# Kernel optimization log

Measured on AMD Instinct MI355X. Metric: run time of the kernel, lower is better.

The kernel has to match this reference:

```python
import jax, jax.numpy as jnp
import numpy as np

N_NODES = 100000
N_EDGES = 1600000
IN_FEATS = 128
OUT_FEATS = 64
NUM_HEADS = 1
K_HOPS = 3
NEG_SLOPE = 0.2


def setup_inputs() -> dict:
    key = jax.random.key(0)
    kf, kw, kl, kr, ks, kd = jax.random.split(key, 6)
    feat = jax.random.normal(kf, (N_NODES, IN_FEATS), dtype=jnp.float32)
    # xavier-normal-ish scaling (gain for relu ~ sqrt(2))
    W = jax.random.normal(kw, (OUT_FEATS * NUM_HEADS, IN_FEATS), dtype=jnp.float32) * np.sqrt(2.0 / (IN_FEATS + OUT_FEATS * NUM_HEADS))
    attn_l = jax.random.normal(kl, (1, NUM_HEADS, OUT_FEATS), dtype=jnp.float32) * 0.1
    attn_r = jax.random.normal(kr, (1, NUM_HEADS, OUT_FEATS), dtype=jnp.float32) * 0.1
    src = jax.random.randint(ks, (N_EDGES,), 0, N_NODES, dtype=jnp.int32)
    dst = jax.random.randint(kd, (N_EDGES,), 0, N_NODES, dtype=jnp.int32)
    return {"feat": feat, "W": W, "attn_l": attn_l, "attn_r": attn_r, "src": src, "dst": dst}


def _edge_softmax(e, dst, n_nodes):
    # e: [E, H, 1]; softmax over incoming edges of each dst node
    emax = jax.ops.segment_max(e, dst, num_segments=n_nodes)  # [N, H, 1]
    ee = jnp.exp(e - emax[dst])
    denom = jax.ops.segment_sum(ee, dst, num_segments=n_nodes)
    return ee / denom[dst]


def reference(feat, W, attn_l, attn_r, src, dst):
    n = feat.shape[0]
    h = (feat @ W.T).reshape(n, NUM_HEADS, OUT_FEATS)  # [N, H, F]
    el = jnp.sum(h * attn_l, axis=-1, keepdims=True)   # [N, H, 1]
    er = jnp.sum(h * attn_r, axis=-1, keepdims=True)   # [N, H, 1]
    e = el[src] + er[dst]                               # [E, H, 1]
    e = jnp.where(e > 0, e, NEG_SLOPE * e)              # leaky_relu
    a = _edge_softmax(e, dst, n)                        # [E, H, 1]

    ones = jnp.ones((src.shape[0],), dtype=feat.dtype)
    out_deg = jax.ops.segment_sum(ones, src, num_segments=n)
    in_deg = jax.ops.segment_sum(ones, dst, num_segments=n)
    out_norm = jnp.power(jnp.clip(out_deg, 1.0, None), -0.5)[:, None, None]  # deg^-0.5
    in_norm = jnp.power(jnp.clip(in_deg, 1.0, None), 0.5)[:, None, None]     # deg^+0.5 (as in source)

    feat_src = h
    for _ in range(K_HOPS):
        feat_src = feat_src * out_norm
        m = feat_src[src] * a                            # [E, H, F]
        feat_src = jax.ops.segment_sum(m, dst, num_segments=n)
        feat_src = feat_src * in_norm
    return feat_src  # [N, H, F]
```

## Files before the change

### kernel.cpp

```cpp
#include <hip/hip_runtime.h>
#include <hip/hip_fp16.h>
#include <math.h>

#define N_NODES 100000
#define N_EDGES 1600000
#define IN_F 128
#define OUT_F 64
#define NEG_SLOPE 0.2f

#define NBUCK 391
#define PB 512
#define EPB (N_EDGES / PB)

#define FS 132

typedef __attribute__((ext_vector_type(8))) short short8;
typedef __attribute__((ext_vector_type(4))) float f32x4;

__device__ __forceinline__ unsigned pack_bf(float f) {
    unsigned u  = __float_as_uint(f);
    unsigned hi = u & 0xffff0000u;
    float    lo = f - __uint_as_float(hi);
    return hi | (__float_as_uint(lo) >> 16);
}

__device__ __forceinline__ void unpack8(uint4 p0, uint4 p1, short8& hi, short8& lo) {
    hi[0] = (short)(p0.x >> 16); lo[0] = (short)(p0.x & 0xffffu);
    hi[1] = (short)(p0.y >> 16); lo[1] = (short)(p0.y & 0xffffu);
    hi[2] = (short)(p0.z >> 16); lo[2] = (short)(p0.z & 0xffffu);
    hi[3] = (short)(p0.w >> 16); lo[3] = (short)(p0.w & 0xffffu);
    hi[4] = (short)(p1.x >> 16); lo[4] = (short)(p1.x & 0xffffu);
    hi[5] = (short)(p1.y >> 16); lo[5] = (short)(p1.y & 0xffffu);
    hi[6] = (short)(p1.z >> 16); lo[6] = (short)(p1.z & 0xffffu);
    hi[7] = (short)(p1.w >> 16); lo[7] = (short)(p1.w & 0xffffu);
}

__global__ __launch_bounds__(256) void k_gemm(
        const float* __restrict__ feat, const float* __restrict__ W,
        const float* __restrict__ attn_l, const float* __restrict__ attn_r,
        __half* __restrict__ h16, float* __restrict__ el, float* __restrict__ er) {
    __shared__ __align__(16) unsigned flds[64 * FS];
    __shared__ __align__(16) unsigned wlds[64 * FS];
    int t = threadIdx.x;
    int n0 = blockIdx.x * 64;

    #pragma unroll
    for (int j = 0; j < 8; ++j) {
        int idx = t + j * 256;
        int row = idx >> 5, k4 = (idx & 31) * 4;
        float4 wv = *(const float4*)&W[row * IN_F + k4];
        unsigned* wp = &wlds[row * FS + k4];
        wp[0] = pack_bf(wv.x); wp[1] = pack_bf(wv.y);
        wp[2] = pack_bf(wv.z); wp[3] = pack_bf(wv.w);
        int g = n0 + row;
        float4 fv = {0.f, 0.f, 0.f, 0.f};
        if (g < N_NODES) fv = *(const float4*)&feat[(size_t)g * IN_F + k4];
        unsigned* fp = &flds[row * FS + k4];
        fp[0] = pack_bf(fv.x); fp[1] = pack_bf(fv.y);
        fp[2] = pack_bf(fv.z); fp[3] = pack_bf(fv.w);
    }
    __syncthreads();

    int lane = t & 63, wv_ = t >> 6;
    int quad = lane >> 4, nl = lane & 15;
    int mrow = wv_ * 16 + nl;

    f32x4 acc[4];
    #pragma unroll
    for (int nt = 0; nt < 4; ++nt) acc[nt] = (f32x4){0.f, 0.f, 0.f, 0.f};

    #pragma unroll
    for (int ks = 0; ks < 4; ++ks) {
        int ko = ks * 32 + quad * 8;
        const uint4* ap = (const uint4*)&flds[mrow * FS + ko];
        uint4 a0 = ap[0], a1 = ap[1];
        short8 ahi, alo; unpack8(a0, a1, ahi, alo);
        #pragma unroll
        for (int nt = 0; nt < 4; ++nt) {
            const uint4* bp = (const uint4*)&wlds[(nt * 16 + nl) * FS + ko];
            uint4 b0 = bp[0], b1 = bp[1];
            short8 bhi, blo; unpack8(b0, b1, bhi, blo);
            acc[nt] = __builtin_amdgcn_mfma_f32_16x16x32_bf16(ahi, bhi, acc[nt], 0, 0, 0);
            acc[nt] = __builtin_amdgcn_mfma_f32_16x16x32_bf16(ahi, blo, acc[nt], 0, 0, 0);
            acc[nt] = __builtin_amdgcn_mfma_f32_16x16x32_bf16(alo, bhi, acc[nt], 0, 0, 0);
        }
    }

    float al4[4], ar4[4];
    #pragma unroll
    for (int nt = 0; nt < 4; ++nt) { al4[nt] = attn_l[nt * 16 + nl]; ar4[nt] = attn_r[nt * 16 + nl]; }
    float elp[4] = {0.f, 0.f, 0.f, 0.f}, erp[4] = {0.f, 0.f, 0.f, 0.f};
    #pragma unroll
    for (int nt = 0; nt < 4; ++nt)
        #pragma unroll
        for (int r = 0; r < 4; ++r) {
            elp[r] += acc[nt][r] * al4[nt];
            erp[r] += acc[nt][r] * ar4[nt];
        }
    #pragma unroll
    for (int off = 1; off <= 8; off <<= 1)
        #pragma unroll
        for (int r = 0; r < 4; ++r) {
            elp[r] += __shfl_xor(elp[r], off);
            erp[r] += __shfl_xor(erp[r], off);
        }
    int gbase = n0 + wv_ * 16 + quad * 4;
    if (nl == 0) {
        #pragma unroll
        for (int r = 0; r < 4; ++r) {
            int g = gbase + r;
            if (g < N_NODES) { el[g] = elp[r]; er[g] = erp[r]; }
        }
    }
    #pragma unroll
    for (int r = 0; r < 4; ++r) {
        int g = gbase + r;
        if (g < N_NODES) {
            #pragma unroll
            for (int nt = 0; nt < 4; ++nt)
                h16[(size_t)g * OUT_F + nt * 16 + nl] = __float2half(acc[nt][r]);
        }
    }
}

__global__ __launch_bounds__(256) void k_hist(
        const int* __restrict__ src, const int* __restrict__ dst,
        int* __restrict__ cntd, int* __restrict__ cnts) {
    __shared__ int hd[NBUCK], hs[NBUCK];
    int t = threadIdx.x, b = blockIdx.x;
    for (int k = t; k < NBUCK; k += 256) { hd[k] = 0; hs[k] = 0; }
    __syncthreads();
    int base = b * EPB;
    for (int i = t; i < EPB; i += 256) {
        atomicAdd(&hd[dst[base + i] >> 8], 1);
        atomicAdd(&hs[src[base + i] >> 8], 1);
    }
    __syncthreads();
    for (int k = t; k < NBUCK; k += 256) {
        cntd[k * PB + b] = hd[k];
        cnts[k * PB + b] = hs[k];
    }
}

__global__ __launch_bounds__(256) void k_colsum(const int* __restrict__ cntd,
                                                const int* __restrict__ cnts,
                                                int* __restrict__ totd,
                                                int* __restrict__ tots) {
    __shared__ int s[256];
    int b = blockIdx.x, t = threadIdx.x;
    const int* m; int* o; int k;
    if (b < NBUCK) { m = cntd; o = totd; k = b; }
    else           { m = cnts; o = tots; k = b - NBUCK; }
    s[t] = m[k * PB + t] + m[k * PB + t + 256];
    __syncthreads();
    for (int d = 128; d; d >>= 1) { if (t < d) s[t] += s[t + d]; __syncthreads(); }
    if (t == 0) o[k] = s[0];
}

__global__ __launch_bounds__(512) void k_bstart(const int* __restrict__ totd,
                                                const int* __restrict__ tots,
                                                int* bstartd, int* bstarts) {
    __shared__ int s[512];
    int t = threadIdx.x;
    int v = (t < NBUCK) ? totd[t] : 0;
    s[t] = v; __syncthreads();
    for (int d = 1; d < 512; d <<= 1) { int a = (t >= d) ? s[t - d] : 0; __syncthreads(); s[t] += a; __syncthreads(); }
    if (t <= NBUCK) bstartd[t] = s[t] - v;
    __syncthreads();
    int v2 = (t < NBUCK) ? tots[t] : 0;
    s[t] = v2; __syncthreads();
    for (int d = 1; d < 512; d <<= 1) { int a = (t >= d) ? s[t - d] : 0; __syncthreads(); s[t] += a; __syncthreads(); }
    if (t <= NBUCK) bstarts[t] = s[t] - v2;
}

__global__ __launch_bounds__(512) void k_blockoff(const int* __restrict__ bstartd,
                                                  const int* __restrict__ bstarts,
                                                  int* cntd, int* cnts) {
    __shared__ int s[512];
    int b = blockIdx.x, t = threadIdx.x;
    int* m; const int* bs; int k;
    if (b < NBUCK) { m = cntd; bs = bstartd; k = b; }
    else           { m = cnts; bs = bstarts; k = b - NBUCK; }
    int c = m[k * PB + t];
    s[t] = c; __syncthreads();
    for (int d = 1; d < 512; d <<= 1) { int a = (t >= d) ? s[t - d] : 0; __syncthreads(); s[t] += a; __syncthreads(); }
    m[k * PB + t] = bs[k] + s[t] - c;
}

__global__ __launch_bounds__(256) void k_scatter_src(
        const int* __restrict__ src, const int* __restrict__ offs,
        unsigned char* __restrict__ tmps) {
    __shared__ int lOffS[NBUCK], lFillS[NBUCK];
    int t = threadIdx.x, b = blockIdx.x;
    for (int k = t; k < NBUCK; k += 256) { lOffS[k] = offs[k * PB + b]; lFillS[k] = 0; }
    __syncthreads();
    int base = b * EPB;
    for (int i = t; i < EPB; i += 256) {
        int sN = src[base + i];
        int ks = sN >> 8;
        int rs = atomicAdd(&lFillS[ks], 1);
        tmps[lOffS[ks] + rs] = (unsigned char)(sN & 255);
    }
}

__global__ __launch_bounds__(256) void k_srccnt(
        const unsigned char* __restrict__ tmps, const int* __restrict__ bstarts,
        float* __restrict__ onorm) {
    __shared__ int cnt[256];
    int k = blockIdx.x, t = threadIdx.x;
    cnt[t] = 0; __syncthreads();
    int base = bstarts[k], end = bstarts[k + 1];
    for (int i = base + t; i < end; i += 256)
        atomicAdd(&cnt[tmps[i]], 1);
    __syncthreads();
    int idx = k * 256 + t;
    if (idx < N_NODES) onorm[idx] = rsqrtf((float)max(cnt[t], 1));
}

__global__ __launch_bounds__(256) void k_scatter3(
        const int* __restrict__ src, const int* __restrict__ dst,
        const float* __restrict__ el, const float* __restrict__ er,
        const int* __restrict__ offd, int2* __restrict__ tmpd) {
    __shared__ int lOffD[NBUCK], lFillD[NBUCK];
    int t = threadIdx.x, b = blockIdx.x;
    for (int k = t; k < NBUCK; k += 256) { lOffD[k] = offd[k * PB + b]; lFillD[k] = 0; }
    __syncthreads();
    int base = b * EPB;
    for (int i = t; i < EPB; i += 256) {
        int e = base + i;
        int sN = src[e], d = dst[e];
        float v = el[sN] + er[d];
        v = (v > 0.f) ? v : NEG_SLOPE * v;
        float pe = __expf(v);
        int kd = d >> 8;
        int rd = atomicAdd(&lFillD[kd], 1);
        int2 rec; rec.x = sN | ((d & 255) << 17); rec.y = __float_as_int(pe);
        tmpd[lOffD[kd] + rd] = rec;
    }
}

__global__ __launch_bounds__(256) void k_bucket(
        const int2* __restrict__ tmp, const int* __restrict__ bstart,
        const float* __restrict__ onorm, float2* __restrict__ csr,
        int* __restrict__ rowstart, float* __restrict__ sigma) {
    __shared__ int   cs[256];
    __shared__ int   excl[256];
    __shared__ int   fill[256];
    __shared__ float dsum[256];
    int k = blockIdx.x, t = threadIdx.x;
    int base = bstart[k], end = bstart[k + 1];
    cs[t] = 0; fill[t] = 0; dsum[t] = 0.f;
    __syncthreads();
    for (int i = base + t; i < end; i += 256)
        atomicAdd(&cs[(tmp[i].x >> 17) & 255], 1);
    __syncthreads();
    int c = cs[t];
    for (int d = 1; d < 256; d <<= 1) {
        int a = (t >= d) ? cs[t - d] : 0;
        __syncthreads();
        cs[t] += a;
        __syncthreads();
    }
    excl[t] = cs[t] - c;
    __syncthreads();
    int idx = k * 256 + t;
    if (idx <= N_NODES) rowstart[idx] = base + excl[t];
    for (int i = base + t; i < end; i += 256) {
        int2 rec = tmp[i];
        int dlow = (rec.x >> 17) & 255;
        int r = atomicAdd(&fill[dlow], 1);
        float pe = __int_as_float(rec.y);
        int sN = rec.x & 131071;
        float2 w;
        w.x = __int_as_float(sN);
        w.y = pe * onorm[sN];
        csr[base + excl[dlow] + r] = w;
        atomicAdd(&dsum[dlow], pe);
    }
    __syncthreads();
    if (idx < N_NODES) {
        float inn = sqrtf((float)max(c, 1));
        sigma[idx] = (c > 0) ? inn / dsum[t] : 0.f;
    }
}

template<typename OT>
__global__ __launch_bounds__(256) void k_spmm(
        const __half* __restrict__ x, const int* __restrict__ rowstart,
        const float2* __restrict__ csr, const float* __restrict__ sigma,
        OT* __restrict__ y) {
    int node = blockIdx.x * 32 + (threadIdx.x >> 3);
    int fl = threadIdx.x & 7;
    if (node >= N_NODES) return;
    int b = rowstart[node], e = rowstart[node + 1];
    float4 a0lo = {0.f, 0.f, 0.f, 0.f}, a0hi = {0.f, 0.f, 0.f, 0.f};
    float4 a1lo = {0.f, 0.f, 0.f, 0.f}, a1hi = {0.f, 0.f, 0.f, 0.f};
    for (int i = b; i < e; i += 8) {
        #pragma unroll
        for (int u = 0; u < 8; ++u) {
            int j = i + u;
            int jc = (j < e) ? j : (e - 1);
            float2 w = csr[jc];
            float vv = (j < e) ? w.y : 0.f;
            unsigned boff = ((unsigned)__float_as_int(w.x) << 7) | ((unsigned)fl << 4);
            uint4 pk = *(const uint4*)((const char*)x + boff);
            float2 f0 = __half22float2(*(__half2*)&pk.x);
            float2 f1 = __half22float2(*(__half2*)&pk.y);
            float2 f2 = __half22float2(*(__half2*)&pk.z);
            float2 f3 = __half22float2(*(__half2*)&pk.w);
            float4& alo = (u & 1) ? a1lo : a0lo;
            float4& ahi = (u & 1) ? a1hi : a0hi;
            alo.x += vv * f0.x; alo.y += vv * f0.y; alo.z += vv * f1.x; alo.w += vv * f1.y;
            ahi.x += vv * f2.x; ahi.y += vv * f2.y; ahi.z += vv * f3.x; ahi.w += vv * f3.y;
        }
    }
    float sg = sigma[node];
    float4 rlo, rhi;
    rlo.x = sg * (a0lo.x + a1lo.x); rlo.y = sg * (a0lo.y + a1lo.y);
    rlo.z = sg * (a0lo.z + a1lo.z); rlo.w = sg * (a0lo.w + a1lo.w);
    rhi.x = sg * (a0hi.x + a1hi.x); rhi.y = sg * (a0hi.y + a1hi.y);
    rhi.z = sg * (a0hi.z + a1hi.z); rhi.w = sg * (a0hi.w + a1hi.w);
    if constexpr (sizeof(OT) == 4) {
        float* yp = (float*)y + (size_t)node * OUT_F + fl * 8;
        *(float4*)yp       = rlo;
        *(float4*)(yp + 4) = rhi;
    } else {
        __half2 p0 = __floats2half2_rn(rlo.x, rlo.y);
        __half2 p1 = __floats2half2_rn(rlo.z, rlo.w);
        __half2 p2 = __floats2half2_rn(rhi.x, rhi.y);
        __half2 p3 = __floats2half2_rn(rhi.z, rhi.w);
        uint4 o;
        o.x = *(unsigned*)&p0; o.y = *(unsigned*)&p1;
        o.z = *(unsigned*)&p2; o.w = *(unsigned*)&p3;
        *(uint4*)((__half*)y + (size_t)node * OUT_F + fl * 8) = o;
    }
}

extern "C" void kernel_launch(void* const* d_in, const int* in_sizes, int n_in,
                              void* d_out, int out_size, void* d_ws, size_t ws_size,
                              hipStream_t stream) {
    const float* feat   = (const float*)d_in[0];
    const float* W      = (const float*)d_in[1];
    const float* attn_l = (const float*)d_in[2];
    const float* attn_r = (const float*)d_in[3];
    const int*   src    = (const int*)d_in[4];
    const int*   dst    = (const int*)d_in[5];
    float* out = (float*)d_out;

    char* p = (char*)d_ws;
    auto alloc = [&](size_t bytes) {
        void* r = (void*)p;
        p += (bytes + 255) & ~(size_t)255;
        return r;
    };
    __half* hbuf = (__half*)alloc((size_t)N_NODES * OUT_F * 2);
    char* r2 = (char*)alloc((size_t)N_EDGES * 8 + (size_t)N_EDGES);
    int2*  tmpd = (int2*)r2;
    unsigned char* tmps = (unsigned char*)(r2 + (size_t)N_EDGES * 8);
    __half* A   = (__half*)r2;

    float2* csr      = (float2*)alloc((size_t)N_EDGES * 8);
    int*    cntd     = (int*)   alloc((size_t)NBUCK * PB * 4);
    int*    cnts     = (int*)   alloc((size_t)NBUCK * PB * 4);
    int*    totd     = (int*)   alloc(NBUCK * 4);
    int*    tots     = (int*)   alloc(NBUCK * 4);
    int*    bstartd  = (int*)   alloc((NBUCK + 1) * 4);
    int*    bstarts  = (int*)   alloc((NBUCK + 1) * 4);
    int*    rowstart = (int*)   alloc((N_NODES + 1) * 4);
    float*  onorm    = (float*) alloc(N_NODES * 4);
    float*  sigma    = (float*) alloc(N_NODES * 4);
    float*  el       = (float*) alloc(N_NODES * 4);
    float*  er       = (float*) alloc(N_NODES * 4);

    const int NGB = (N_NODES + 63) / 64;

    k_gemm       <<<NGB,       256, 0, stream>>>(feat, W, attn_l, attn_r, hbuf, el, er);
    k_hist       <<<PB,        256, 0, stream>>>(src, dst, cntd, cnts);
    k_colsum     <<<2 * NBUCK, 256, 0, stream>>>(cntd, cnts, totd, tots);
    k_bstart     <<<1,         512, 0, stream>>>(totd, tots, bstartd, bstarts);
    k_blockoff   <<<2 * NBUCK, 512, 0, stream>>>(bstartd, bstarts, cntd, cnts);
    k_scatter_src<<<PB,        256, 0, stream>>>(src, cnts, tmps);
    k_srccnt     <<<NBUCK,     256, 0, stream>>>(tmps, bstarts, onorm);
    k_scatter3   <<<PB,        256, 0, stream>>>(src, dst, el, er, cntd, tmpd);
    k_bucket     <<<NBUCK,     256, 0, stream>>>(tmpd, bstartd, onorm, csr, rowstart, sigma);

    const int nb_spmm = (N_NODES + 31) / 32;
    k_spmm<__half><<<nb_spmm, 256, 0, stream>>>(hbuf, rowstart, csr, sigma, A);
    k_spmm<__half><<<nb_spmm, 256, 0, stream>>>(A,    rowstart, csr, sigma, hbuf);
    k_spmm<float> <<<nb_spmm, 256, 0, stream>>>(hbuf, rowstart, csr, sigma, out);
}
```

Before: 299.1 us.

## Compute source out-degrees with global atomics instead of a bucket sort

Replaces the two-pass source bucketing (src histogram, offsets, byte scatter, per-bucket count) with direct global atomicAdd per edge into a per-node degree array that is zeroed by a memset. The out-norm rsqrt is then computed inline in k_bucket from the degree array. This drops two kernels and half of the colsum, bstart and blockoff work, in exchange for 1.6M scattered global atomics, which may contend.

```diff
diff --git a/kernel.cpp b/kernel.cpp
--- a/kernel.cpp
+++ b/kernel.cpp
@@ -125,96 +125,49 @@
 
 __global__ __launch_bounds__(256) void k_hist(
         const int* __restrict__ src, const int* __restrict__ dst,
-        int* __restrict__ cntd, int* __restrict__ cnts) {
-    __shared__ int hd[NBUCK], hs[NBUCK];
+        int* __restrict__ cntd, int* __restrict__ degs) {
+    __shared__ int hd[NBUCK];
     int t = threadIdx.x, b = blockIdx.x;
-    for (int k = t; k < NBUCK; k += 256) { hd[k] = 0; hs[k] = 0; }
+    for (int k = t; k < NBUCK; k += 256) hd[k] = 0;
     __syncthreads();
     int base = b * EPB;
     for (int i = t; i < EPB; i += 256) {
         atomicAdd(&hd[dst[base + i] >> 8], 1);
-        atomicAdd(&hs[src[base + i] >> 8], 1);
-    }
-    __syncthreads();
-    for (int k = t; k < NBUCK; k += 256) {
+        atomicAdd(&degs[src[base + i]], 1);
+    }
+    __syncthreads();
+    for (int k = t; k < NBUCK; k += 256)
         cntd[k * PB + b] = hd[k];
-        cnts[k * PB + b] = hs[k];
-    }
 }
 
 __global__ __launch_bounds__(256) void k_colsum(const int* __restrict__ cntd,
-                                                const int* __restrict__ cnts,
-                                                int* __restrict__ totd,
-                                                int* __restrict__ tots) {
+                                                int* __restrict__ totd) {
     __shared__ int s[256];
-    int b = blockIdx.x, t = threadIdx.x;
-    const int* m; int* o; int k;
-    if (b < NBUCK) { m = cntd; o = totd; k = b; }
-    else           { m = cnts; o = tots; k = b - NBUCK; }
-    s[t] = m[k * PB + t] + m[k * PB + t + 256];
+    int k = blockIdx.x, t = threadIdx.x;
+    s[t] = cntd[k * PB + t] + cntd[k * PB + t + 256];
     __syncthreads();
     for (int d = 128; d; d >>= 1) { if (t < d) s[t] += s[t + d]; __syncthreads(); }
-    if (t == 0) o[k] = s[0];
+    if (t == 0) totd[k] = s[0];
 }
 
 __global__ __launch_bounds__(512) void k_bstart(const int* __restrict__ totd,
-                                                const int* __restrict__ tots,
-                                                int* bstartd, int* bstarts) {
+                                                int* bstartd) {
     __shared__ int s[512];
     int t = threadIdx.x;
     int v = (t < NBUCK) ? totd[t] : 0;
     s[t] = v; __syncthreads();
     for (int d = 1; d < 512; d <<= 1) { int a = (t >= d) ? s[t - d] : 0; __syncthreads(); s[t] += a; __syncthreads(); }
     if (t <= NBUCK) bstartd[t] = s[t] - v;
-    __syncthreads();
-    int v2 = (t < NBUCK) ? tots[t] : 0;
-    s[t] = v2; __syncthreads();
-    for (int d = 1; d < 512; d <<= 1) { int a = (t >= d) ? s[t - d] : 0; __syncthreads(); s[t] += a; __syncthreads(); }
-    if (t <= NBUCK) bstarts[t] = s[t] - v2;
 }
 
 __global__ __launch_bounds__(512) void k_blockoff(const int* __restrict__ bstartd,
-                                                  const int* __restrict__ bstarts,
-                                                  int* cntd, int* cnts) {
+                                                  int* cntd) {
     __shared__ int s[512];
-    int b = blockIdx.x, t = threadIdx.x;
-    int* m; const int* bs; int k;
-    if (b < NBUCK) { m = cntd; bs = bstartd; k = b; }
-    else           { m = cnts; bs = bstarts; k = b - NBUCK; }
-    int c = m[k * PB + t];
+    int k = blockIdx.x, t = threadIdx.x;
+    int c = cntd[k * PB + t];
     s[t] = c; __syncthreads();
     for (int d = 1; d < 512; d <<= 1) { int a = (t >= d) ? s[t - d] : 0; __syncthreads(); s[t] += a; __syncthreads(); }
-    m[k * PB + t] = bs[k] + s[t] - c;
-}
-
-__global__ __launch_bounds__(256) void k_scatter_src(
-        const int* __restrict__ src, const int* __restrict__ offs,
-        unsigned char* __restrict__ tmps) {
-    __shared__ int lOffS[NBUCK], lFillS[NBUCK];
-    int t = threadIdx.x, b = blockIdx.x;
-    for (int k = t; k < NBUCK; k += 256) { lOffS[k] = offs[k * PB + b]; lFillS[k] = 0; }
-    __syncthreads();
-    int base = b * EPB;
-    for (int i = t; i < EPB; i += 256) {
-        int sN = src[base + i];
-        int ks = sN >> 8;
-        int rs = atomicAdd(&lFillS[ks], 1);
-        tmps[lOffS[ks] + rs] = (unsigned char)(sN & 255);
-    }
-}
-
-__global__ __launch_bounds__(256) void k_srccnt(
-        const unsigned char* __restrict__ tmps, const int* __restrict__ bstarts,
-        float* __restrict__ onorm) {
-    __shared__ int cnt[256];
-    int k = blockIdx.x, t = threadIdx.x;
-    cnt[t] = 0; __syncthreads();
-    int base = bstarts[k], end = bstarts[k + 1];
-    for (int i = base + t; i < end; i += 256)
-        atomicAdd(&cnt[tmps[i]], 1);
-    __syncthreads();
-    int idx = k * 256 + t;
-    if (idx < N_NODES) onorm[idx] = rsqrtf((float)max(cnt[t], 1));
+    cntd[k * PB + t] = bstartd[k] + s[t] - c;
 }
 
 __global__ __launch_bounds__(256) void k_scatter3(
@@ -241,7 +194,7 @@
 
 __global__ __launch_bounds__(256) void k_bucket(
         const int2* __restrict__ tmp, const int* __restrict__ bstart,
-        const float* __restrict__ onorm, float2* __restrict__ csr,
+        const int* __restrict__ degs, float2* __restrict__ csr,
         int* __restrict__ rowstart, float* __restrict__ sigma) {
     __shared__ int   cs[256];
     __shared__ int   excl[256];
@@ -273,7 +226,7 @@
         int sN = rec.x & 131071;
         float2 w;
         w.x = __int_as_float(sN);
-        w.y = pe * onorm[sN];
+        w.y = pe * rsqrtf((float)max(degs[sN], 1));
         csr[base + excl[dlow] + r] = w;
         atomicAdd(&dsum[dlow], pe);
     }
@@ -354,35 +307,31 @@
         return r;
     };
     __half* hbuf = (__half*)alloc((size_t)N_NODES * OUT_F * 2);
-    char* r2 = (char*)alloc((size_t)N_EDGES * 8 + (size_t)N_EDGES);
+    char* r2 = (char*)alloc((size_t)N_EDGES * 8);
     int2*  tmpd = (int2*)r2;
-    unsigned char* tmps = (unsigned char*)(r2 + (size_t)N_EDGES * 8);
     __half* A   = (__half*)r2;
 
     float2* csr      = (float2*)alloc((size_t)N_EDGES * 8);
     int*    cntd     = (int*)   alloc((size_t)NBUCK * PB * 4);
-    int*    cnts     = (int*)   alloc((size_t)NBUCK * PB * 4);
     int*    totd     = (int*)   alloc(NBUCK * 4);
-    int*    tots     = (int*)   alloc(NBUCK * 4);
     int*    bstartd  = (int*)   alloc((NBUCK + 1) * 4);
-    int*    bstarts  = (int*)   alloc((NBUCK + 1) * 4);
     int*    rowstart = (int*)   alloc((N_NODES + 1) * 4);
-    float*  onorm    = (float*) alloc(N_NODES * 4);
+    int*    degs     = (int*)   alloc(N_NODES * 4);
     float*  sigma    = (float*) alloc(N_NODES * 4);
     float*  el       = (float*) alloc(N_NODES * 4);
     float*  er       = (float*) alloc(N_NODES * 4);
 
     const int NGB = (N_NODES + 63) / 64;
 
-    k_gemm       <<<NGB,       256, 0, stream>>>(feat, W, attn_l, attn_r, hbuf, el, er);
-    k_hist       <<<PB,        256, 0, stream>>>(src, dst, cntd, cnts);
-    k_colsum     <<<2 * NBUCK, 256, 0, stream>>>(cntd, cnts, totd, tots);
-    k_bstart     <<<1,         512, 0, stream>>>(totd, tots, bstartd, bstarts);
-    k_blockoff   <<<2 * NBUCK, 512, 0, stream>>>(bstartd, bstarts, cntd, cnts);
-    k_scatter_src<<<PB,        256, 0, stream>>>(src, cnts, tmps);
-    k_srccnt     <<<NBUCK,     256, 0, stream>>>(tmps, bstarts, onorm);
-    k_scatter3   <<<PB,        256, 0, stream>>>(src, dst, el, er, cntd, tmpd);
-    k_bucket     <<<NBUCK,     256, 0, stream>>>(tmpd, bstartd, onorm, csr, rowstart, sigma);
+    hipMemsetAsync(degs, 0, (size_t)N_NODES * 4, stream);
+
+    k_gemm     <<<NGB,   256, 0, stream>>>(feat, W, attn_l, attn_r, hbuf, el, er);
+    k_hist     <<<PB,    256, 0, stream>>>(src, dst, cntd, degs);
+    k_colsum   <<<NBUCK, 256, 0, stream>>>(cntd, totd);
+    k_bstart   <<<1,     512, 0, stream>>>(totd, bstartd);
+    k_blockoff <<<NBUCK, 512, 0, stream>>>(bstartd, cntd);
+    k_scatter3 <<<PB,    256, 0, stream>>>(src, dst, el, er, cntd, tmpd);
+    k_bucket   <<<NBUCK, 256, 0, stream>>>(tmpd, bstartd, degs, csr, rowstart, sigma);
 
     const int nb_spmm = (N_NODES + 31) / 32;
     k_spmm<__half><<<nb_spmm, 256, 0, stream>>>(hbuf, rowstart, csr, sigma, A);
```

After: 333.8 us. 1.12x slower.
